# Performance work log

Measured on AMD Instinct MI355X. Metric: run time of the kernel, lower is better.

Reference implementation:

```python
import jax, jax.numpy as jnp
import numpy as np

N = 50000
E = 800000
DIM_IN, DIM_H, DIM_OUT, HEADS = 128, 8, 32, 15
NEG_SLOPE = 0.2  # PyG GATv2Conv default


def gatv2_layer(x, src, dst, Wl, Wr, att, bias, num_nodes):
    """PyG GATv2Conv (share_weights=False, concat=True) with self-loops already in src/dst.
    x: [N, F_in]; Wl/Wr: [F_in, H*C]; att: [H, C]; bias: [H*C].
    """
    H, C = att.shape
    xl = (x @ Wl).reshape(-1, H, C)  # source transform [N,H,C]
    xr = (x @ Wr).reshape(-1, H, C)  # target transform [N,H,C]
    s = jax.nn.leaky_relu(xl[src] + xr[dst], negative_slope=NEG_SLOPE)  # [E,H,C]
    e = jnp.einsum('ehc,hc->eh', s, att)  # attention logits [E,H]
    # numerically-stable segment softmax over incoming edges of each dst node
    emax = jax.ops.segment_max(e, dst, num_segments=num_nodes)  # [N,H]
    ee = jnp.exp(e - emax[dst])
    denom = jax.ops.segment_sum(ee, dst, num_segments=num_nodes)  # [N,H]
    alpha = ee / denom[dst]  # self-loops guarantee denom > 0
    out = jax.ops.segment_sum(alpha[:, :, None] * xl[src], dst, num_segments=num_nodes)  # [N,H,C]
    return out.reshape(num_nodes, H * C) + bias


def setup_inputs() -> dict:
    key = jax.random.key(0)
    ks = jax.random.split(key, 10)
    x = jax.random.normal(ks[0], (N, DIM_IN), dtype=jnp.float32)
    edge_index = jax.random.randint(ks[1], (2, E), 0, N, dtype=jnp.int64)
    g1 = 1.0 / np.sqrt(DIM_IN)
    g2 = 1.0 / np.sqrt(DIM_H * HEADS)
    return {
        'x': x,
        'edge_index': edge_index,
        'W1l': jax.random.normal(ks[2], (DIM_IN, HEADS * DIM_H), dtype=jnp.float32) * g1,
        'W1r': jax.random.normal(ks[3], (DIM_IN, HEADS * DIM_H), dtype=jnp.float32) * g1,
        'att1': jax.random.normal(ks[4], (HEADS, DIM_H), dtype=jnp.float32) * (1.0 / np.sqrt(DIM_H)),
        'b1': jnp.zeros((HEADS * DIM_H,), dtype=jnp.float32),
        'W2l': jax.random.normal(ks[5], (HEADS * DIM_H, DIM_OUT), dtype=jnp.float32) * g2,
        'W2r': jax.random.normal(ks[6], (HEADS * DIM_H, DIM_OUT), dtype=jnp.float32) * g2,
        'att2': jax.random.normal(ks[7], (1, DIM_OUT), dtype=jnp.float32) * (1.0 / np.sqrt(DIM_OUT)),
        'b2': jnp.zeros((DIM_OUT,), dtype=jnp.float32),
    }


def reference(x, edge_index, W1l, W1r, att1, b1, W2l, W2r, att2, b2):
    n = x.shape[0]
    loops = jnp.arange(n, dtype=edge_index.dtype)
    src = jnp.concatenate([edge_index[0], loops])  # PyG add_self_loops=True
    dst = jnp.concatenate([edge_index[1], loops])
    h = gatv2_layer(x, src, dst, W1l, W1r, att1, b1, n)  # [N, HEADS*DIM_H]
    h = jax.nn.elu(h)
    # dropout(p=0.3) is identity in eval mode
    h = gatv2_layer(h, src, dst, W2l, W2r, att2, b2, n)  # heads=1 -> [N, DIM_OUT]
    return h, jax.nn.log_softmax(h, axis=1)
```

## Files before the change

### kernel.cpp

```cpp
#include <hip/hip_runtime.h>
#include <math.h>

namespace {
constexpr int NN  = 50000;
constexpr int EE  = 800000;
constexpr int FIN = 128;
constexpr int HC1 = 120;
constexpr int F2  = 32;
constexpr int MT  = NN / 16;
constexpr int CAP = 64;
constexpr int NBIN = 64;
constexpr int BINW = 782;
constexpr int BINCAP = 16384;
constexpr int TILE = 4096;
constexpr int ABLK = (EE + TILE - 1) / TILE;
}

typedef __attribute__((ext_vector_type(8))) short bf16x8;
typedef __attribute__((ext_vector_type(4))) float f32x4;

template<int CTRL>
__device__ __forceinline__ float dppf(float x) {
    return __int_as_float(__builtin_amdgcn_mov_dpp(__float_as_int(x), CTRL, 0xF, 0xF, true));
}
__device__ __forceinline__ float quad_sum(float x) {
    x += dppf<0xB1>(x);
    x += dppf<0x4E>(x);
    return x;
}
template<int MASK>
__device__ __forceinline__ float swz_add(float x) {
    return x + __int_as_float(__builtin_amdgcn_ds_swizzle(__float_as_int(x), (MASK << 10) | 0x1F));
}
template<int MASK>
__device__ __forceinline__ float swz_max(float x) {
    return fmaxf(x, __int_as_float(__builtin_amdgcn_ds_swizzle(__float_as_int(x), (MASK << 10) | 0x1F)));
}

__device__ __forceinline__ unsigned short f2bf(float f) {
    unsigned int u = __float_as_uint(f);
    unsigned int r = (u + 0x7fffu + ((u >> 16) & 1u)) >> 16;
    return (unsigned short)r;
}
__device__ __forceinline__ float2 bf2f2(unsigned int u) {
    return make_float2(__uint_as_float(u << 16), __uint_as_float(u & 0xffff0000u));
}

__device__ __forceinline__ void edge_sd_raw(const unsigned int* __restrict__ raw, int is64,
                                            int e, int& s, int& d) {
    s = is64 ? (int)raw[2 * (size_t)e] : (int)raw[e];
    d = is64 ? (int)raw[2 * (size_t)(EE + e)] : (int)raw[EE + e];
}

__global__ void prep_init_kernel(const unsigned int* __restrict__ raw,
                                 const float* __restrict__ W1l, const float* __restrict__ W1r,
                                 const float* __restrict__ W2l, const float* __restrict__ W2r,
                                 unsigned short* __restrict__ Bf1, unsigned short* __restrict__ Bf2,
                                 int* __restrict__ cursor, int* __restrict__ flag) {
    int tid = blockIdx.x * blockDim.x + threadIdx.x;
    if (blockIdx.x == 0 && threadIdx.x < 64) {
        int t = threadIdx.x;
        unsigned int hi = raw[2 * t + 1];
        unsigned long long ball = __ballot(hi == 0u);
        if (t == 0) *flag = (ball == ~0ULL) ? 1 : 0;
    }
    if (tid < 4096) {
        int t = tid >> 8, lane = tid & 63;
        int kb = (tid >> 6) & 3;
        int k0 = kb * 32 + (lane >> 4) * 8;
        int n = (t & 7) * 16 + (lane & 15);
        const float* W = (t < 8) ? W1l : W1r;
        #pragma unroll
        for (int j = 0; j < 8; ++j)
            Bf1[(size_t)tid * 8 + j] = (n < HC1) ? f2bf(W[(k0 + j) * HC1 + n]) : (unsigned short)0;
    } else if (tid < 5120) {
        int id = tid - 4096;
        int t = id >> 8, lane = id & 63;
        int kb = (id >> 6) & 3;
        int k0 = kb * 32 + (lane >> 4) * 8;
        int nl = (t & 1) * 16 + (lane & 15);
        const float* W = (t < 2) ? W2l : W2r;
        #pragma unroll
        for (int j = 0; j < 8; ++j) {
            int k = k0 + j;
            Bf2[(size_t)id * 8 + j] = (k < HC1) ? f2bf(W[k * F2 + nl]) : (unsigned short)0;
        }
    } else if (tid >= 8192 && tid < 8192 + NBIN) {
        cursor[tid - 8192] = 0;
    }
}

__global__ void __launch_bounds__(256) binA_kernel(
    const unsigned int* __restrict__ raw, const int* __restrict__ flag,
    int* __restrict__ cursor, uint2* __restrict__ binbuf) {
    __shared__ int lcnt[NBIN];
    __shared__ int lbase[NBIN];
    __shared__ int lcnt2[NBIN];
    int tid = threadIdx.x;
    int e0 = blockIdx.x * TILE;
    int is64 = *flag;
    if (tid < NBIN) { lcnt[tid] = 0; lcnt2[tid] = 0; }
    __syncthreads();
    #pragma unroll
    for (int i = 0; i < TILE / 256; ++i) {
        int e = e0 + i * 256 + tid;
        if (e < EE) {
            int d = is64 ? (int)raw[2 * (size_t)(EE + e)] : (int)raw[EE + e];
            atomicAdd(&lcnt[d / BINW], 1);
        }
    }
    __syncthreads();
    if (tid < NBIN) {
        int c = lcnt[tid];
        lbase[tid] = (c > 0) ? atomicAdd(&cursor[tid], c) : 0;
    }
    __syncthreads();
    #pragma unroll
    for (int i = 0; i < TILE / 256; ++i) {
        int e = e0 + i * 256 + tid;
        if (e < EE) {
            int s, d;
            edge_sd_raw(raw, is64, e, s, d);
            int bin = d / BINW;
            int pos = lbase[bin] + atomicAdd(&lcnt2[bin], 1);
            if (pos < BINCAP) binbuf[(size_t)bin * BINCAP + pos] = make_uint2((unsigned)s, (unsigned)d);
        }
    }
}

__global__ void __launch_bounds__(1024) binB_kernel(
    const int* __restrict__ cursor, const uint2* __restrict__ binbuf,
    int* __restrict__ cnt, unsigned short* __restrict__ bucket) {
    __shared__ int lcnt[BINW];
    int g = blockIdx.x;
    int tid = threadIdx.x;
    int ng0 = g * BINW;
    if (tid < BINW) lcnt[tid] = 0;
    __syncthreads();
    int m = min(cursor[g], BINCAP);
    for (int base = 0; base < m; base += 1024) {
        int i = base + tid;
        if (i < m) {
            uint2 u = binbuf[(size_t)g * BINCAP + i];
            int d = (int)u.y;
            int pos = atomicAdd(&lcnt[d - ng0], 1);
            if (pos < CAP) bucket[(size_t)d * CAP + pos] = (unsigned short)u.x;
        }
    }
    __syncthreads();
    int nn = min(BINW, NN - ng0);
    if (tid < nn) cnt[ng0 + tid] = lcnt[tid];
}

__global__ void __launch_bounds__(256) gemm1_mfma_kernel(
    const float* __restrict__ x, const unsigned short* __restrict__ Bf,
    unsigned short* __restrict__ xlb, float* __restrict__ xr) {
    int wave = threadIdx.x >> 6, lane = threadIdx.x & 63;
    int mt = blockIdx.x * 4 + wave;
    if (mt >= MT) return;
    int n0 = mt * 16;
    int lr = lane & 15, kg = lane >> 4;
    const float* xrow = x + (size_t)(n0 + lr) * FIN + kg * 8;
    bf16x8 a[4];
    #pragma unroll
    for (int ko = 0; ko < 4; ++ko) {
        float4 lo = *(const float4*)(xrow + ko * 32);
        float4 hi = *(const float4*)(xrow + ko * 32 + 4);
        union { unsigned int u[4]; bf16x8 v; } cv;
        cv.u[0] = f2bf(lo.x) | ((unsigned int)f2bf(lo.y) << 16);
        cv.u[1] = f2bf(lo.z) | ((unsigned int)f2bf(lo.w) << 16);
        cv.u[2] = f2bf(hi.x) | ((unsigned int)f2bf(hi.y) << 16);
        cv.u[3] = f2bf(hi.z) | ((unsigned int)f2bf(hi.w) << 16);
        a[ko] = cv.v;
    }
    const bf16x8* bp = (const bf16x8*)Bf + lane;
    f32x4 acc[16];
    #pragma unroll
    for (int t = 0; t < 16; ++t) acc[t] = (f32x4){0.f, 0.f, 0.f, 0.f};
    #pragma unroll
    for (int t = 0; t < 16; ++t) {
        bf16x8 b0 = bp[(t * 4 + 0) * 64];
        bf16x8 b1 = bp[(t * 4 + 1) * 64];
        bf16x8 b2 = bp[(t * 4 + 2) * 64];
        bf16x8 b3 = bp[(t * 4 + 3) * 64];
        acc[t] = __builtin_amdgcn_mfma_f32_16x16x32_bf16(a[0], b0, acc[t], 0, 0, 0);
        acc[t] = __builtin_amdgcn_mfma_f32_16x16x32_bf16(a[1], b1, acc[t], 0, 0, 0);
        acc[t] = __builtin_amdgcn_mfma_f32_16x16x32_bf16(a[2], b2, acc[t], 0, 0, 0);
        acc[t] = __builtin_amdgcn_mfma_f32_16x16x32_bf16(a[3], b3, acc[t], 0, 0, 0);
    }
    #pragma unroll
    for (int t = 0; t < 8; ++t) {
        int cg = t * 16 + lr;
        if (cg < HC1) {
            #pragma unroll
            for (int r = 0; r < 4; ++r)
                xlb[(size_t)(n0 + kg * 4 + r) * HC1 + cg] = f2bf(acc[t][r]);
        }
    }
    #pragma unroll
    for (int t = 8; t < 16; ++t) {
        int cg = (t - 8) * 16 + lr;
        if (cg < HC1) {
            #pragma unroll
            for (int r = 0; r < 4; ++r)
                xr[(size_t)(n0 + kg * 4 + r) * HC1 + cg] = acc[t][r];
        }
    }
}

__global__ void __launch_bounds__(256) fused1_kernel(
    const unsigned short* __restrict__ bucket, const int* __restrict__ cnt,
    const unsigned short* __restrict__ xlb, const float* __restrict__ xr,
    const float* __restrict__ att, const float* __restrict__ b1,
    unsigned int* __restrict__ hout) {
    __shared__ int s_src[4][64];
    int wave = threadIdx.x >> 6;
    int lane = threadIdx.x & 63;
    int n = blockIdx.x * 4 + wave;
    bool act = lane < 60;
    int c0 = act ? 2 * lane : 0;
    float2 xrv = *(const float2*)(xr + (size_t)n * HC1 + c0);
    float2 atv = *(const float2*)(att + c0);
    int deg = min(cnt[n], CAP);
    int srcv = (lane < deg) ? (int)bucket[(size_t)n * CAP + lane] : 0;
    s_src[wave][lane] = srcv;
    float s, o0, o1;
    {
        unsigned int ua = *(const unsigned int*)(xlb + (size_t)n * HC1 + c0);
        float2 ra = bf2f2(ua);
        float t0 = ra.x + xrv.x; t0 = fmaxf(t0, 0.2f * t0);
        float t1 = ra.y + xrv.y; t1 = fmaxf(t1, 0.2f * t1);
        float pa = quad_sum(atv.x * t0 + atv.y * t1);
        float ea = __expf(fminf(pa, 60.f));
        s = ea; o0 = ea * ra.x; o1 = ea * ra.y;
    }
    for (int j = 0; j < deg; j += 2) {
        int2 ss = *(const int2*)&s_src[wave][j];
        unsigned int ua = *(const unsigned int*)(xlb + (size_t)ss.x * HC1 + c0);
        unsigned int ub = *(const unsigned int*)(xlb + (size_t)ss.y * HC1 + c0);
        float2 ra = bf2f2(ua);
        float2 rb = bf2f2(ub);
        float t0, t1;
        t0 = ra.x + xrv.x; t0 = fmaxf(t0, 0.2f * t0);
        t1 = ra.y + xrv.y; t1 = fmaxf(t1, 0.2f * t1);
        float pa = atv.x * t0 + atv.y * t1;
        t0 = rb.x + xrv.x; t0 = fmaxf(t0, 0.2f * t0);
        t1 = rb.y + xrv.y; t1 = fmaxf(t1, 0.2f * t1);
        float pb = atv.x * t0 + atv.y * t1;
        pa = quad_sum(pa);
        pb = quad_sum(pb);
        float ea = __expf(fminf(pa, 60.f));
        float eb = (j + 1 < deg) ? __expf(fminf(pb, 60.f)) : 0.f;
        s += ea + eb;
        o0 = fmaf(eb, rb.x, fmaf(ea, ra.x, o0));
        o1 = fmaf(eb, rb.y, fmaf(ea, ra.y, o1));
    }
    unsigned int packed = 0u;
    if (act) {
        float inv = 1.0f / s;
        float2 bv = *(const float2*)(b1 + c0);
        float v0 = o0 * inv + bv.x;
        float v1 = o1 * inv + bv.y;
        v0 = v0 > 0.f ? v0 : __expf(v0) - 1.f;
        v1 = v1 > 0.f ? v1 : __expf(v1) - 1.f;
        packed = (unsigned int)f2bf(v0) | ((unsigned int)f2bf(v1) << 16);
    }
    hout[(size_t)n * 64 + lane] = packed;
}

__global__ void __launch_bounds__(256) gemm2_mfma_kernel(
    const unsigned short* __restrict__ hb, const unsigned short* __restrict__ Bf,
    unsigned short* __restrict__ xl2b, float* __restrict__ xr2) {
    int wave = threadIdx.x >> 6, lane = threadIdx.x & 63;
    int mt = blockIdx.x * 4 + wave;
    if (mt >= MT) return;
    int n0 = mt * 16;
    int lr = lane & 15, kg = lane >> 4;
    const unsigned short* ab = hb + (size_t)(n0 + lr) * FIN + kg * 8;
    bf16x8 a0 = *(const bf16x8*)(ab);
    bf16x8 a1 = *(const bf16x8*)(ab + 32);
    bf16x8 a2 = *(const bf16x8*)(ab + 64);
    bf16x8 a3 = *(const bf16x8*)(ab + 96);
    const bf16x8* bp = (const bf16x8*)Bf + lane;
    f32x4 acc[4];
    #pragma unroll
    for (int t = 0; t < 4; ++t) acc[t] = (f32x4){0.f, 0.f, 0.f, 0.f};
    #pragma unroll
    for (int t = 0; t < 4; ++t) {
        bf16x8 b0 = bp[(t * 4 + 0) * 64];
        bf16x8 b1 = bp[(t * 4 + 1) * 64];
        bf16x8 b2 = bp[(t * 4 + 2) * 64];
        bf16x8 b3 = bp[(t * 4 + 3) * 64];
        acc[t] = __builtin_amdgcn_mfma_f32_16x16x32_bf16(a0, b0, acc[t], 0, 0, 0);
        acc[t] = __builtin_amdgcn_mfma_f32_16x16x32_bf16(a1, b1, acc[t], 0, 0, 0);
        acc[t] = __builtin_amdgcn_mfma_f32_16x16x32_bf16(a2, b2, acc[t], 0, 0, 0);
        acc[t] = __builtin_amdgcn_mfma_f32_16x16x32_bf16(a3, b3, acc[t], 0, 0, 0);
    }
    #pragma unroll
    for (int t = 0; t < 2; ++t) {
        int cg = t * 16 + lr;
        #pragma unroll
        for (int r = 0; r < 4; ++r)
            xl2b[(size_t)(n0 + kg * 4 + r) * F2 + cg] = f2bf(acc[t][r]);
    }
    #pragma unroll
    for (int t = 2; t < 4; ++t) {
        int cg = (t - 2) * 16 + lr;
        #pragma unroll
        for (int r = 0; r < 4; ++r)
            xr2[(size_t)(n0 + kg * 4 + r) * F2 + cg] = acc[t][r];
    }
}

__global__ void __launch_bounds__(256) fused2_kernel(
    const unsigned short* __restrict__ bucket, const int* __restrict__ cnt,
    const unsigned short* __restrict__ xl2b, const float* __restrict__ xr2,
    const float* __restrict__ att2, const float* __restrict__ b2,
    float* __restrict__ out) {
    __shared__ int s_src[4][64];
    int wave = threadIdx.x >> 6;
    int lane = threadIdx.x & 63;
    int n = blockIdx.x * 4 + wave;
    int grp = lane >> 4;
    int cl = lane & 15;
    int c0 = 2 * cl;
    float2 xrv = *(const float2*)(xr2 + (size_t)n * F2 + c0);
    float2 atv = *(const float2*)(att2 + c0);
    int deg = min(cnt[n], CAP);
    int srcv = (lane < deg) ? (int)bucket[(size_t)n * CAP + lane] : 0;
    s_src[wave][lane] = srcv;
    float s, o0, o1;
    {
        unsigned int u = *(const unsigned int*)(xl2b + (size_t)n * F2 + c0);
        float2 r = bf2f2(u);
        float t0 = r.x + xrv.x; t0 = fmaxf(t0, 0.2f * t0);
        float t1 = r.y + xrv.y; t1 = fmaxf(t1, 0.2f * t1);
        float p = atv.x * t0 + atv.y * t1;
        p = quad_sum(p);
        p = swz_add<4>(p);
        p = swz_add<8>(p);
        float e = (grp == 0) ? __expf(fminf(p, 60.f)) : 0.f;
        s = e; o0 = e * r.x; o1 = e * r.y;
    }
    for (int j = 0; j < deg; j += 4) {
        int myj = j + grp;
        int src = s_src[wave][min(myj, 63)];
        bool val = myj < deg;
        unsigned int u = *(const unsigned int*)(xl2b + (size_t)src * F2 + c0);
        float2 r = bf2f2(u);
        float t0 = r.x + xrv.x; t0 = fmaxf(t0, 0.2f * t0);
        float t1 = r.y + xrv.y; t1 = fmaxf(t1, 0.2f * t1);
        float p = atv.x * t0 + atv.y * t1;
        p = quad_sum(p);
        p = swz_add<4>(p);
        p = swz_add<8>(p);
        float e = val ? __expf(fminf(p, 60.f)) : 0.f;
        s += e;
        o0 = fmaf(e, r.x, o0);
        o1 = fmaf(e, r.y, o1);
    }
    s  = swz_add<16>(s);   s  += __shfl_xor(s, 32);
    o0 = swz_add<16>(o0);  o0 += __shfl_xor(o0, 32);
    o1 = swz_add<16>(o1);  o1 += __shfl_xor(o1, 32);
    float2 bv = *(const float2*)(b2 + c0);
    float inv = 1.0f / s;
    float v0 = o0 * inv + bv.x;
    float v1 = o1 * inv + bv.y;
    float mm = fmaxf(v0, v1);
    mm = fmaxf(mm, dppf<0xB1>(mm));
    mm = fmaxf(mm, dppf<0x4E>(mm));
    mm = swz_max<4>(mm);
    mm = swz_max<8>(mm);
    float se = __expf(v0 - mm) + __expf(v1 - mm);
    se += dppf<0xB1>(se);
    se += dppf<0x4E>(se);
    se = swz_add<4>(se);
    se = swz_add<8>(se);
    float lse = mm + __logf(se);
    if (lane < 16) {
        *(float2*)(out + (size_t)n * F2 + c0) = make_float2(v0, v1);
        *(float2*)(out + (size_t)NN * F2 + (size_t)n * F2 + c0) =
            make_float2(v0 - lse, v1 - lse);
    }
}

extern "C" void kernel_launch(void* const* d_in, const int* in_sizes, int n_in,
                              void* d_out, int out_size, void* d_ws, size_t ws_size,
                              hipStream_t stream) {
    const float* x    = (const float*)d_in[0];
    const unsigned int* ei_raw = (const unsigned int*)d_in[1];
    const float* W1l  = (const float*)d_in[2];
    const float* W1r  = (const float*)d_in[3];
    const float* att1 = (const float*)d_in[4];
    const float* b1   = (const float*)d_in[5];
    const float* W2l  = (const float*)d_in[6];
    const float* W2r  = (const float*)d_in[7];
    const float* att2 = (const float*)d_in[8];
    const float* b2   = (const float*)d_in[9];
    float* out = (float*)d_out;

    char* ws = (char*)d_ws;
    float* XR1           = (float*)ws;          ws += (size_t)NN * HC1 * 4;
    unsigned int* HHb    = (unsigned int*)ws;   ws += (size_t)NN * 64 * 4;
    float* XR2           = (float*)ws;          ws += (size_t)NN * F2 * 4;
    unsigned short* XL1b = (unsigned short*)ws; ws += (size_t)NN * HC1 * 2;
    unsigned short* XL2b = (unsigned short*)ws; ws += (size_t)NN * F2 * 2;
    unsigned short* BF1  = (unsigned short*)ws; ws += 16 * 4 * 64 * 8 * 2;
    unsigned short* BF2  = (unsigned short*)ws; ws += 4 * 4 * 64 * 8 * 2;
    unsigned short* BUCKET = (unsigned short*)ws; ws += (size_t)NN * CAP * 2;
    uint2* BINBUF = (uint2*)ws;                 ws += (size_t)NBIN * BINCAP * 8;
    int* CURSOR = (int*)ws;                     ws += NBIN * 4;
    int* CNT    = (int*)ws;                     ws += (size_t)NN * 4;
    int* FLAG   = (int*)ws;

    prep_init_kernel<<<64, 256, 0, stream>>>(ei_raw, W1l, W1r, W2l, W2r,
                                             BF1, BF2, CURSOR, FLAG);

    binA_kernel<<<ABLK, 256, 0, stream>>>(ei_raw, FLAG, CURSOR, BINBUF);
    binB_kernel<<<NBIN, 1024, 0, stream>>>(CURSOR, BINBUF, CNT, BUCKET);

    gemm1_mfma_kernel<<<(MT + 3) / 4, 256, 0, stream>>>(x, BF1, XL1b, XR1);
    fused1_kernel<<<NN / 4, 256, 0, stream>>>(BUCKET, CNT, XL1b, XR1, att1, b1, HHb);

    gemm2_mfma_kernel<<<(MT + 3) / 4, 256, 0, stream>>>(
        (const unsigned short*)HHb, BF2, XL2b, XR2);
    fused2_kernel<<<NN / 4, 256, 0, stream>>>(BUCKET, CNT, XL2b, XR2, att2, b2, out);
}
```

Before: 218.8 us.

## Pack bin entries to 32 bits, sort buckets by source chunk, store xr as bf16

Each edge in the bin buffer is now a single 32-bit word (src<<16 | dst) instead of a uint2, which halves the traffic of the binning passes. binB now runs two passes: it counts per destination and per source chunk (four chunks), takes a prefix sum, then scatters. This orders each node's neighbour list by source region, which should improve locality of the later gathers, at the cost of reading the bin buffer twice. xr for both layers is also stored as bf16 instead of fp32, which cuts write and read bandwidth but lowers the precision of the attention logits.

```diff
diff --git a/kernel.cpp b/kernel.cpp
--- a/kernel.cpp
+++ b/kernel.cpp
@@ -14,6 +14,7 @@
 constexpr int BINCAP = 16384;
 constexpr int TILE = 4096;
 constexpr int ABLK = (EE + TILE - 1) / TILE;
+constexpr int CHUNKW = 12500;
 }
 
 typedef __attribute__((ext_vector_type(8))) short bf16x8;
@@ -44,12 +45,6 @@
 }
 __device__ __forceinline__ float2 bf2f2(unsigned int u) {
     return make_float2(__uint_as_float(u << 16), __uint_as_float(u & 0xffff0000u));
-}
-
-__device__ __forceinline__ void edge_sd_raw(const unsigned int* __restrict__ raw, int is64,
-                                            int e, int& s, int& d) {
-    s = is64 ? (int)raw[2 * (size_t)e] : (int)raw[e];
-    d = is64 ? (int)raw[2 * (size_t)(EE + e)] : (int)raw[EE + e];
 }
 
 __global__ void prep_init_kernel(const unsigned int* __restrict__ raw,
@@ -92,7 +87,7 @@
 
 __global__ void __launch_bounds__(256) binA_kernel(
     const unsigned int* __restrict__ raw, const int* __restrict__ flag,
-    int* __restrict__ cursor, uint2* __restrict__ binbuf) {
+    int* __restrict__ cursor, unsigned int* __restrict__ binbuf) {
     __shared__ int lcnt[NBIN];
     __shared__ int lbase[NBIN];
     __shared__ int lcnt2[NBIN];
@@ -119,42 +114,55 @@
     for (int i = 0; i < TILE / 256; ++i) {
         int e = e0 + i * 256 + tid;
         if (e < EE) {
-            int s, d;
-            edge_sd_raw(raw, is64, e, s, d);
-            int bin = d / BINW;
+            unsigned int s = is64 ? raw[2 * (size_t)e] : raw[e];
+            unsigned int d = is64 ? raw[2 * (size_t)(EE + e)] : raw[EE + e];
+            int bin = (int)d / BINW;
             int pos = lbase[bin] + atomicAdd(&lcnt2[bin], 1);
-            if (pos < BINCAP) binbuf[(size_t)bin * BINCAP + pos] = make_uint2((unsigned)s, (unsigned)d);
+            if (pos < BINCAP) binbuf[(size_t)bin * BINCAP + pos] = (s << 16) | d;
         }
     }
 }
 
 __global__ void __launch_bounds__(1024) binB_kernel(
-    const int* __restrict__ cursor, const uint2* __restrict__ binbuf,
+    const int* __restrict__ cursor, const unsigned int* __restrict__ binbuf,
     int* __restrict__ cnt, unsigned short* __restrict__ bucket) {
-    __shared__ int lcnt[BINW];
+    __shared__ int lc[BINW * 4];
     int g = blockIdx.x;
     int tid = threadIdx.x;
     int ng0 = g * BINW;
-    if (tid < BINW) lcnt[tid] = 0;
+    for (int i = tid; i < BINW * 4; i += 1024) lc[i] = 0;
     __syncthreads();
     int m = min(cursor[g], BINCAP);
-    for (int base = 0; base < m; base += 1024) {
-        int i = base + tid;
-        if (i < m) {
-            uint2 u = binbuf[(size_t)g * BINCAP + i];
-            int d = (int)u.y;
-            int pos = atomicAdd(&lcnt[d - ng0], 1);
-            if (pos < CAP) bucket[(size_t)d * CAP + pos] = (unsigned short)u.x;
-        }
-    }
-    __syncthreads();
-    int nn = min(BINW, NN - ng0);
-    if (tid < nn) cnt[ng0 + tid] = lcnt[tid];
+    const unsigned int* bb = binbuf + (size_t)g * BINCAP;
+    for (int i = tid; i < m; i += 1024) {
+        unsigned int u = bb[i];
+        int d = (int)(u & 0xffffu);
+        int s = (int)(u >> 16);
+        atomicAdd(&lc[(d - ng0) * 4 + s / CHUNKW], 1);
+    }
+    __syncthreads();
+    if (tid < BINW) {
+        int c0 = lc[tid * 4], c1 = lc[tid * 4 + 1], c2 = lc[tid * 4 + 2], c3 = lc[tid * 4 + 3];
+        lc[tid * 4] = 0;
+        lc[tid * 4 + 1] = c0;
+        lc[tid * 4 + 2] = c0 + c1;
+        lc[tid * 4 + 3] = c0 + c1 + c2;
+        int n = ng0 + tid;
+        if (n < NN) cnt[n] = min(c0 + c1 + c2 + c3, CAP);
+    }
+    __syncthreads();
+    for (int i = tid; i < m; i += 1024) {
+        unsigned int u = bb[i];
+        int d = (int)(u & 0xffffu);
+        int s = (int)(u >> 16);
+        int pos = atomicAdd(&lc[(d - ng0) * 4 + s / CHUNKW], 1);
+        if (pos < CAP) bucket[(size_t)d * CAP + pos] = (unsigned short)s;
+    }
 }
 
 __global__ void __launch_bounds__(256) gemm1_mfma_kernel(
     const float* __restrict__ x, const unsigned short* __restrict__ Bf,
-    unsigned short* __restrict__ xlb, float* __restrict__ xr) {
+    unsigned short* __restrict__ xlb, unsigned short* __restrict__ xrb) {
     int wave = threadIdx.x >> 6, lane = threadIdx.x & 63;
     int mt = blockIdx.x * 4 + wave;
     if (mt >= MT) return;
@@ -189,28 +197,20 @@
         acc[t] = __builtin_amdgcn_mfma_f32_16x16x32_bf16(a[3], b3, acc[t], 0, 0, 0);
     }
     #pragma unroll
-    for (int t = 0; t < 8; ++t) {
-        int cg = t * 16 + lr;
+    for (int t = 0; t < 16; ++t) {
+        unsigned short* outp = (t < 8) ? xlb : xrb;
+        int cg = (t & 7) * 16 + lr;
         if (cg < HC1) {
             #pragma unroll
             for (int r = 0; r < 4; ++r)
-                xlb[(size_t)(n0 + kg * 4 + r) * HC1 + cg] = f2bf(acc[t][r]);
-        }
-    }
-    #pragma unroll
-    for (int t = 8; t < 16; ++t) {
-        int cg = (t - 8) * 16 + lr;
-        if (cg < HC1) {
-            #pragma unroll
-            for (int r = 0; r < 4; ++r)
-                xr[(size_t)(n0 + kg * 4 + r) * HC1 + cg] = acc[t][r];
+                outp[(size_t)(n0 + kg * 4 + r) * HC1 + cg] = f2bf(acc[t][r]);
         }
     }
 }
 
 __global__ void __launch_bounds__(256) fused1_kernel(
     const unsigned short* __restrict__ bucket, const int* __restrict__ cnt,
-    const unsigned short* __restrict__ xlb, const float* __restrict__ xr,
+    const unsigned short* __restrict__ xlb, const unsigned short* __restrict__ xrb,
     const float* __restrict__ att, const float* __restrict__ b1,
     unsigned int* __restrict__ hout) {
     __shared__ int s_src[4][64];
@@ -219,7 +219,7 @@
     int n = blockIdx.x * 4 + wave;
     bool act = lane < 60;
     int c0 = act ? 2 * lane : 0;
-    float2 xrv = *(const float2*)(xr + (size_t)n * HC1 + c0);
+    float2 xrv = bf2f2(*(const unsigned int*)(xrb + (size_t)n * HC1 + c0));
     float2 atv = *(const float2*)(att + c0);
     int deg = min(cnt[n], CAP);
     int srcv = (lane < deg) ? (int)bucket[(size_t)n * CAP + lane] : 0;
@@ -270,7 +270,7 @@
 
 __global__ void __launch_bounds__(256) gemm2_mfma_kernel(
     const unsigned short* __restrict__ hb, const unsigned short* __restrict__ Bf,
-    unsigned short* __restrict__ xl2b, float* __restrict__ xr2) {
+    unsigned short* __restrict__ xl2b, unsigned short* __restrict__ xr2b) {
     int wave = threadIdx.x >> 6, lane = threadIdx.x & 63;
     int mt = blockIdx.x * 4 + wave;
     if (mt >= MT) return;
@@ -297,24 +297,18 @@
         acc[t] = __builtin_amdgcn_mfma_f32_16x16x32_bf16(a3, b3, acc[t], 0, 0, 0);
     }
     #pragma unroll
-    for (int t = 0; t < 2; ++t) {
-        int cg = t * 16 + lr;
+    for (int t = 0; t < 4; ++t) {
+        unsigned short* outp = (t < 2) ? xl2b : xr2b;
+        int cg = (t & 1) * 16 + lr;
         #pragma unroll
         for (int r = 0; r < 4; ++r)
-            xl2b[(size_t)(n0 + kg * 4 + r) * F2 + cg] = f2bf(acc[t][r]);
-    }
-    #pragma unroll
-    for (int t = 2; t < 4; ++t) {
-        int cg = (t - 2) * 16 + lr;
-        #pragma unroll
-        for (int r = 0; r < 4; ++r)
-            xr2[(size_t)(n0 + kg * 4 + r) * F2 + cg] = acc[t][r];
+            outp[(size_t)(n0 + kg * 4 + r) * F2 + cg] = f2bf(acc[t][r]);
     }
 }
 
 __global__ void __launch_bounds__(256) fused2_kernel(
     const unsigned short* __restrict__ bucket, const int* __restrict__ cnt,
-    const unsigned short* __restrict__ xl2b, const float* __restrict__ xr2,
+    const unsigned short* __restrict__ xl2b, const unsigned short* __restrict__ xr2b,
     const float* __restrict__ att2, const float* __restrict__ b2,
     float* __restrict__ out) {
     __shared__ int s_src[4][64];
@@ -324,7 +318,7 @@
     int grp = lane >> 4;
     int cl = lane & 15;
     int c0 = 2 * cl;
-    float2 xrv = *(const float2*)(xr2 + (size_t)n * F2 + c0);
+    float2 xrv = bf2f2(*(const unsigned int*)(xr2b + (size_t)n * F2 + c0));
     float2 atv = *(const float2*)(att2 + c0);
     int deg = min(cnt[n], CAP);
     int srcv = (lane < deg) ? (int)bucket[(size_t)n * CAP + lane] : 0;
@@ -400,15 +394,15 @@
     float* out = (float*)d_out;
 
     char* ws = (char*)d_ws;
-    float* XR1           = (float*)ws;          ws += (size_t)NN * HC1 * 4;
+    unsigned short* XR1b = (unsigned short*)ws; ws += (size_t)NN * HC1 * 2;
     unsigned int* HHb    = (unsigned int*)ws;   ws += (size_t)NN * 64 * 4;
-    float* XR2           = (float*)ws;          ws += (size_t)NN * F2 * 4;
+    unsigned short* XR2b = (unsigned short*)ws; ws += (size_t)NN * F2 * 2;
     unsigned short* XL1b = (unsigned short*)ws; ws += (size_t)NN * HC1 * 2;
     unsigned short* XL2b = (unsigned short*)ws; ws += (size_t)NN * F2 * 2;
     unsigned short* BF1  = (unsigned short*)ws; ws += 16 * 4 * 64 * 8 * 2;
     unsigned short* BF2  = (unsigned short*)ws; ws += 4 * 4 * 64 * 8 * 2;
     unsigned short* BUCKET = (unsigned short*)ws; ws += (size_t)NN * CAP * 2;
-    uint2* BINBUF = (uint2*)ws;                 ws += (size_t)NBIN * BINCAP * 8;
+    unsigned int* BINBUF = (unsigned int*)ws;   ws += (size_t)NBIN * BINCAP * 4;
     int* CURSOR = (int*)ws;                     ws += NBIN * 4;
     int* CNT    = (int*)ws;                     ws += (size_t)NN * 4;
     int* FLAG   = (int*)ws;
@@ -419,10 +413,10 @@
     binA_kernel<<<ABLK, 256, 0, stream>>>(ei_raw, FLAG, CURSOR, BINBUF);
     binB_kernel<<<NBIN, 1024, 0, stream>>>(CURSOR, BINBUF, CNT, BUCKET);
 
-    gemm1_mfma_kernel<<<(MT + 3) / 4, 256, 0, stream>>>(x, BF1, XL1b, XR1);
-    fused1_kernel<<<NN / 4, 256, 0, stream>>>(BUCKET, CNT, XL1b, XR1, att1, b1, HHb);
+    gemm1_mfma_kernel<<<(MT + 3) / 4, 256, 0, stream>>>(x, BF1, XL1b, XR1b);
+    fused1_kernel<<<NN / 4, 256, 0, stream>>>(BUCKET, CNT, XL1b, XR1b, att1, b1, HHb);
 
     gemm2_mfma_kernel<<<(MT + 3) / 4, 256, 0, stream>>>(
-        (const unsigned short*)HHb, BF2, XL2b, XR2);
-    fused2_kernel<<<NN / 4, 256, 0, stream>>>(BUCKET, CNT, XL2b, XR2, att2, b2, out);
-}
+        (const unsigned short*)HHb, BF2, XL2b, XR2b);
+    fused2_kernel<<<NN / 4, 256, 0, stream>>>(BUCKET, CNT, XL2b, XR2b, att2, b2, out);
+}
```

Measured after the change: 214.0 us. 1.02x faster.
